# Performance work log

Measured on AMD Instinct MI355X. Metric: run time of the kernel, lower is better.

Reference implementation:

```python
import jax, jax.numpy as jnp
import numpy as np

B, Hc, Wc, C, NH, SR, WS = 4, 64, 64, 256, 8, 2, 4
N = Hc * Wc


def _window_partition(x, ws, H, W):
    # x: (B, h, N, d) -> (B*h*nWin, ws*ws, d)
    Bb, h, _, d = x.shape
    x = x.reshape(Bb * h, H // ws, ws, W // ws, ws, d)
    x = x.transpose(0, 1, 3, 2, 4, 5)
    return x.reshape(-1, ws * ws, d)


def _window_reverse(win, ws, H, W, head):
    nwin = (H // ws) * (W // ws)
    Bh = win.shape[0] // nwin
    x = win.reshape(Bh, H // ws, W // ws, ws, ws, -1).transpose(0, 1, 3, 2, 4, 5).reshape(Bh, H, W, -1)
    Bb = Bh // head
    x = x.reshape(Bb, head, H, W, -1).transpose(0, 2, 3, 1, 4)  # heads interleave into channels
    return x.reshape(Bb, H * W, -1)


def _layernorm(x, w, b):
    m = x.mean(-1, keepdims=True)
    v = x.var(-1, keepdims=True)
    return (x - m) / jnp.sqrt(v + 1e-5) * w + b


def setup_inputs() -> dict:
    key = jax.random.key(0)
    ks = jax.random.split(key, 16)
    lin = lambda k, i, o: 0.02 * jax.random.normal(k, (i, o), jnp.float32)
    inp = {
        'x': jax.random.normal(ks[0], (B, N, C), jnp.float32),
        'q1_w': lin(ks[1], C, C // 2), 'q1_b': jnp.zeros((C // 2,), jnp.float32),
        'kv1_w': lin(ks[2], C, C), 'kv1_b': jnp.zeros((C,), jnp.float32),
        'q2_w': lin(ks[3], C, C // 2), 'q2_b': jnp.zeros((C // 2,), jnp.float32),
        'kv2_w': lin(ks[4], C, C), 'kv2_b': jnp.zeros((C,), jnp.float32),
        'lepe_w': lin(ks[5], C, C), 'lepe_b': jnp.zeros((C,), jnp.float32),
        'lepe_conv_w': jnp.sqrt(2.0 / 9.0) * jax.random.normal(ks[6], (C, 1, 3, 3), jnp.float32),
        'lepe_conv_b': jnp.zeros((C,), jnp.float32),
        'sr_w': jnp.sqrt(2.0 / (SR * SR * C)) * jax.random.normal(ks[7], (C, C, SR, SR), jnp.float32),
        'sr_b': jnp.zeros((C,), jnp.float32),
        'norm_w': jnp.ones((C,), jnp.float32), 'norm_b': jnp.zeros((C,), jnp.float32),
        'proj_w': lin(ks[8], C, C), 'proj_b': jnp.zeros((C,), jnp.float32),
        'H': Hc, 'W': Wc,
    }
    return inp


def reference(x, q1_w, q1_b, kv1_w, kv1_b, q2_w, q2_b, kv2_w, kv2_b,
              lepe_w, lepe_b, lepe_conv_w, lepe_conv_b, sr_w, sr_b,
              norm_w, norm_b, proj_w, proj_b, H, W):
    Bb, Nn, Cc = x.shape
    h2 = NH // 2
    d = Cc // NH
    sr = sr_w.shape[-1]
    scale = d ** -0.5
    ws = WS

    # lepe: linear -> depthwise 3x3 conv
    l = (x @ lepe_w + lepe_b).transpose(0, 2, 1).reshape(Bb, Cc, H, W)
    l = jax.lax.conv_general_dilated(l, lepe_conv_w, (1, 1), ((1, 1), (1, 1)),
                                     dimension_numbers=('NCHW', 'OIHW', 'NCHW'),
                                     feature_group_count=Cc) + lepe_conv_b[None, :, None, None]
    lepe = l.reshape(Bb, Cc, Nn).transpose(0, 2, 1)

    # branch 1: spatial-reduction global attention
    q1 = (x @ q1_w + q1_b).reshape(Bb, Nn, h2, d).transpose(0, 2, 1, 3)
    x_img = x.transpose(0, 2, 1).reshape(Bb, Cc, H, W)
    xs = jax.lax.conv_general_dilated(x_img, sr_w, (sr, sr), 'VALID',
                                      dimension_numbers=('NCHW', 'OIHW', 'NCHW')) + sr_b[None, :, None, None]
    N1 = (H // sr) * (W // sr)
    xs = xs.reshape(Bb, Cc, N1).transpose(0, 2, 1)
    xs = jax.nn.gelu(_layernorm(xs, norm_w, norm_b), approximate=False)
    kv1 = (xs @ kv1_w + kv1_b).reshape(Bb, N1, 2, h2, d).transpose(2, 0, 3, 1, 4)
    k1, v1 = kv1[0], kv1[1]
    attn1 = jax.nn.softmax(jnp.einsum('bhnd,bhmd->bhnm', q1, k1) * scale, axis=-1)
    x1 = jnp.einsum('bhnm,bhmd->bnhd', attn1, v1).reshape(Bb, Nn, Cc // 2)
    g = jax.lax.stop_gradient(attn1).mean(1).mean(1).reshape(Bb, H // sr, W // sr)
    g = jnp.repeat(jnp.repeat(g, sr, axis=1), sr, axis=2)  # nearest upsample to (B,H,W)

    # branch 2: Swin-style windowed attention (window 4)
    q2 = (x @ q2_w + q2_b).reshape(Bb, Nn, h2, d).transpose(0, 2, 1, 3)
    kv2 = (x @ kv2_w + kv2_b).reshape(Bb, Nn, 2, h2, d).transpose(2, 0, 3, 1, 4)
    k2, v2 = kv2[0], kv2[1]
    q2w = _window_partition(q2, ws, H, W)
    k2w = _window_partition(k2, ws, H, W)
    v2w = _window_partition(v2, ws, H, W)
    attn2 = jax.nn.softmax(jnp.einsum('wnd,wmd->wnm', q2w, k2w) * scale, axis=-1)
    x2 = jnp.einsum('wnm,wmd->wnd', attn2, v2w)
    x2 = _window_reverse(x2, ws, H, W, h2)
    nwin = (H // ws) * (W // ws)
    lm = jax.lax.stop_gradient(attn2).reshape(Bb, h2, nwin, ws * ws, ws * ws).mean(1).mean(2)
    lm = lm.reshape(Bb, H // ws, W // ws, ws, ws).transpose(0, 1, 3, 2, 4).reshape(Bb, H, W)

    out = jnp.concatenate([x1, x2], axis=-1)
    p = (out + lepe) @ proj_w + proj_b
    out = p + p  # proj_drop is identity at p=0.0, so x = drop(p) + p = 2p

    mask = lm + g
    mask1 = mask.reshape(Bb, H * W)
    mask2 = mask.transpose(0, 2, 1).reshape(Bb, H * W)
    return out, mask1, mask2
```

## Files before the change

kernel.cpp:

```cpp
#include <hip/hip_runtime.h>
#include <hip/hip_bf16.h>
#include <math.h>

typedef __hip_bfloat16 bf16;
typedef __attribute__((ext_vector_type(8))) short bf16x8;
typedef __attribute__((ext_vector_type(4))) short bf16x4;
typedef __attribute__((ext_vector_type(4))) float f32x4;

__device__ __forceinline__ float b2f(bf16 v) { return __bfloat162float(v); }
__device__ __forceinline__ bf16  f2b(float v) { return __float2bfloat16(v); }
__device__ __forceinline__ float s2f(short v) { return __uint_as_float(((unsigned)(unsigned short)v) << 16); }

__device__ __forceinline__ void gl_lds16(const void* g, void* l)
{
    __builtin_amdgcn_global_load_lds(
        (const __attribute__((address_space(1))) void*)g,
        (__attribute__((address_space(3))) void*)l, 16, 0, 0);
}

__global__ void detect_dtype(const void* x, int* flag)
{
    __shared__ int cnt;
    if (threadIdx.x == 0) cnt = 0;
    __syncthreads();
    const unsigned* w = (const unsigned*)x;
    int sane = 0;
    for (int i = threadIdx.x; i < 2048; i += 256) {
        unsigned lo = (w[i] & 0xFFFFu) << 16;
        float v = __uint_as_float(lo);
        float a = fabsf(v);
        if (v == 0.f || (a > 1e-8f && a < 1e4f)) sane++;
    }
    atomicAdd(&cnt, sane);
    __syncthreads();
    if (threadIdx.x == 0) *flag = (cnt < 1640) ? 1 : 0;
}

struct AllArgs {
    const void* x; bf16* cx;
    const void* srw;  bf16* srwT;
    const void* dww;  bf16* dwT;
    const void* psrc[10]; bf16* pdst[10]; int pn[10];
    const void* wsrc[6]; bf16* wdst[6]; int wN[6]; int wblkoff[7];
    float* gbuf;
};
__global__ void convert_all(AllArgs a, const int* __restrict__ flag)
{
    int blk = blockIdx.x, t = threadIdx.x;
    int fl = *flag;
    if (blk < 4096) {
        int i = blk * 256 + t;
        if (fl) {
            float4 v = ((const float4*)a.x)[i];
            bf16 tmp[4];
            tmp[0] = f2b(v.x); tmp[1] = f2b(v.y); tmp[2] = f2b(v.z); tmp[3] = f2b(v.w);
            *(bf16x4*)&a.cx[i * 4] = *(bf16x4*)tmp;
        } else {
            ((bf16x4*)a.cx)[i] = ((const bf16x4*)a.x)[i];
        }
    } else if (blk < 5120) {
        int o = (blk - 4096) * 256 + t;
        int co = o >> 10, kg = o & 1023;
        int e = kg >> 8, ci = kg & 255;
        int si = co * 1024 + ci * 4 + e;
        float v = fl ? ((const float*)a.srw)[si] : s2f(((const short*)a.srw)[si]);
        a.srwT[o] = f2b(v);
    } else if (blk < 5129) {
        int o = (blk - 5120) * 256 + t;
        if (o >= 2304) return;
        int k = o >> 8, c = o & 255;
        float v = fl ? ((const float*)a.dww)[c * 9 + k] : s2f(((const short*)a.dww)[c * 9 + k]);
        a.dwT[o] = f2b(v);
    } else if (blk < 5139) {
        int bi = blk - 5129;
        int n = a.pn[bi];
        const void* s = a.psrc[bi];
        bf16* d = a.pdst[bi];
        for (int i = t; i < n; i += 256)
            d[i] = fl ? f2b(((const float*)s)[i]) : f2b(s2f(((const short*)s)[i]));
    } else if (blk < 6419) {
        int wblk = blk - 5139;
        int ti = 0;
        while (wblk >= a.wblkoff[ti + 1]) ++ti;
        int o = (wblk - a.wblkoff[ti]) * 256 + t;
        int n = o >> 8, k = o & 255;
        int N = a.wN[ti];
        float v = fl ? ((const float*)a.wsrc[ti])[k * N + n]
                     : s2f(((const short*)a.wsrc[ti])[k * N + n]);
        a.wdst[ti][o] = f2b(v);
    } else {
        for (int i = t; i < 4096; i += 256) a.gbuf[i] = 0.f;
    }
}

__device__ __forceinline__ void qkv_body(
    int bx, int by, char* smem,
    const bf16* __restrict__ A, const bf16* __restrict__ WT, const bf16* __restrict__ bias,
    bf16* __restrict__ Cl, bf16* __restrict__ Cq1, bf16* __restrict__ Cq2, bf16* __restrict__ Ckv2)
{
    char* As = smem;
    char* Bs = smem + 8192;
    int t = threadIdx.x;
    int m0 = bx * 128, ybase = by * 128;
    int w = t >> 6, l = t & 63, lane16 = l & 15, quad = l >> 4;
    int wr = w >> 1, wc = w & 1;

    int oph0 = w * 2048 + l * 16;
    int oph1 = oph0 + 1024;
    int olog0 = oph0 ^ (((oph0 >> 7) & 3) << 4);
    int olog1 = oph1 ^ (((oph1 >> 7) & 3) << 4);
    int row0 = olog0 >> 6, ce0 = (olog0 & 63) >> 1;
    int row1 = olog1 >> 6, ce1 = (olog1 & 63) >> 1;
    char* asb0 = As + w * 2048; char* asb1 = asb0 + 1024;
    char* bsb0 = Bs + w * 2048; char* bsb1 = bsb0 + 1024;

    f32x4 acc[4][4] = {};
    for (int k0 = 0; k0 < 256; k0 += 32) {
        gl_lds16(&A[(size_t)(m0 + row0) * 256 + k0 + ce0], asb0);
        gl_lds16(&A[(size_t)(m0 + row1) * 256 + k0 + ce1], asb1);
        gl_lds16(&WT[(size_t)(ybase + row0) * 256 + k0 + ce0], bsb0);
        gl_lds16(&WT[(size_t)(ybase + row1) * 256 + k0 + ce1], bsb1);
        __syncthreads();
        bf16x8 a[4], b[4];
        #pragma unroll
        for (int i = 0; i < 4; ++i) {
            int ra = wr * 64 + i * 16 + lane16;
            int oa = (ra << 6) + (quad << 4);
            oa ^= (((oa >> 7) & 3) << 4);
            a[i] = *(const bf16x8*)(As + oa);
            int rb = wc * 64 + i * 16 + lane16;
            int ob = (rb << 6) + (quad << 4);
            ob ^= (((ob >> 7) & 3) << 4);
            b[i] = *(const bf16x8*)(Bs + ob);
        }
        #pragma unroll
        for (int i = 0; i < 4; ++i)
            #pragma unroll
            for (int j = 0; j < 4; ++j)
                acc[i][j] = __builtin_amdgcn_mfma_f32_16x16x32_bf16(a[i], b[j], acc[i][j], 0, 0, 0);
        __syncthreads();
    }
    bf16* C; int N, cbase;
    if (ybase < 256)      { C = Cl;   N = 256; cbase = ybase; }
    else if (ybase < 384) { C = Cq1;  N = 128; cbase = ybase - 256; }
    else if (ybase < 512) { C = Cq2;  N = 128; cbase = ybase - 384; }
    else                  { C = Ckv2; N = 256; cbase = ybase - 512; }
    float mult = (ybase >= 256 && ybase < 512)
               ? (0.17677669529663687f * 1.4426950408889634f) : 1.f;
    #pragma unroll
    for (int j = 0; j < 4; ++j) {
        int gcol = ybase + wc * 64 + j * 16 + lane16;
        float bv = b2f(bias[gcol]);
        int col = cbase + wc * 64 + j * 16 + lane16;
        #pragma unroll
        for (int i = 0; i < 4; ++i)
            #pragma unroll
            for (int r = 0; r < 4; ++r) {
                int row = m0 + wr * 64 + i * 16 + quad * 4 + r;
                C[(size_t)row * N + col] = f2b((acc[i][j][r] + bv) * mult);
            }
    }
}

__device__ __forceinline__ void sr_body(
    int bx, int by, char* smem,
    const bf16* __restrict__ x, const bf16* __restrict__ WT,
    const bf16* __restrict__ bias, bf16* __restrict__ C)
{
    bf16 (*As)[40] = (bf16(*)[40])smem;
    bf16 (*Bs)[40] = (bf16(*)[40])(smem + 5120);
    int t = threadIdx.x;
    int m0 = bx * 64, n0 = by * 64;
    int w = t >> 6, l = t & 63, lane16 = l & 15, quad = l >> 4;
    int sr = t >> 2, sc = (t & 3) * 8;
    int brow = m0 + sr;
    int b = brow >> 10, p = brow & 1023;
    int pi = p >> 5, pj = p & 31;
    f32x4 acc[4] = {};
    for (int k0 = 0; k0 < 1024; k0 += 32) {
        int kg = k0 + sc;
        int e = kg >> 8, ci = kg & 255;
        int di = e >> 1, dj = e & 1;
        int n = (2 * pi + di) * 64 + 2 * pj + dj;
        *(bf16x8*)&As[sr][sc] = *(const bf16x8*)&x[(size_t)((b << 12) + n) * 256 + ci];
        *(bf16x8*)&Bs[sr][sc] = *(const bf16x8*)&WT[(size_t)(n0 + sr) * 1024 + kg];
        __syncthreads();
        bf16x8 a = *(const bf16x8*)&As[w * 16 + lane16][quad * 8];
        #pragma unroll
        for (int ct = 0; ct < 4; ++ct) {
            bf16x8 bb = *(const bf16x8*)&Bs[ct * 16 + lane16][quad * 8];
            acc[ct] = __builtin_amdgcn_mfma_f32_16x16x32_bf16(a, bb, acc[ct], 0, 0, 0);
        }
        __syncthreads();
    }
    #pragma unroll
    for (int ct = 0; ct < 4; ++ct) {
        int col = n0 + ct * 16 + lane16;
        float bv = b2f(bias[col]);
        #pragma unroll
        for (int r = 0; r < 4; ++r) {
            int row = m0 + w * 16 + quad * 4 + r;
            C[(size_t)row * 256 + col] = f2b(acc[ct][r] + bv);
        }
    }
}

__global__ __launch_bounds__(256) void fuseA(
    const bf16* __restrict__ cx, const bf16* __restrict__ wTqkv, const bf16* __restrict__ bcat,
    bf16* __restrict__ Cl, bf16* __restrict__ Cq1, bf16* __restrict__ Cq2, bf16* __restrict__ Ckv2,
    const bf16* __restrict__ srwT, const bf16* __restrict__ srb, bf16* __restrict__ xs_pre)
{
    __shared__ __align__(16) char smem[16384];
    int idx = blockIdx.x;
    int g = idx >> 2, r3 = idx & 3;
    if (r3 < 3) {
        int q = g * 3 + r3;
        qkv_body(q & 127, q >> 7, smem, cx, wTqkv, bcat, Cl, Cq1, Cq2, Ckv2);
    } else {
        sr_body(g & 63, g >> 6, smem, cx, srwT, srb, xs_pre);
    }
}

__device__ __forceinline__ void ln_body(
    int blk,
    const bf16* __restrict__ xin, const bf16* __restrict__ nw,
    const bf16* __restrict__ nb, bf16* __restrict__ xout)
{
    int w = threadIdx.x >> 6, lane = threadIdx.x & 63;
    int r = blk * 4 + w;
    bf16x4 xv = *(const bf16x4*)&xin[(size_t)r * 256 + lane * 4];
    float v[4];
    #pragma unroll
    for (int j = 0; j < 4; ++j) v[j] = s2f(xv[j]);
    float s = v[0] + v[1] + v[2] + v[3];
    #pragma unroll
    for (int o = 1; o <= 32; o <<= 1) s += __shfl_xor(s, o);
    float mean = s * (1.f / 256.f);
    float ss = 0.f;
    #pragma unroll
    for (int j = 0; j < 4; ++j) { float d = v[j] - mean; ss += d * d; }
    #pragma unroll
    for (int o = 1; o <= 32; o <<= 1) ss += __shfl_xor(ss, o);
    float inv = rsqrtf(ss * (1.f / 256.f) + 1e-5f);
    bf16x4 wv = *(const bf16x4*)&nw[lane * 4];
    bf16x4 bv = *(const bf16x4*)&nb[lane * 4];
    bf16 ov[4];
    #pragma unroll
    for (int j = 0; j < 4; ++j) {
        float y = (v[j] - mean) * inv * s2f(wv[j]) + s2f(bv[j]);
        ov[j] = f2b(0.5f * y * (1.f + erff(y * 0.70710678118654752f)));
    }
    *(bf16x4*)&xout[(size_t)r * 256 + lane * 4] = *(bf16x4*)ov;
}

__device__ __forceinline__ void dw_body(
    int blk,
    const bf16* __restrict__ lin, const bf16* __restrict__ dwT,
    const bf16* __restrict__ bias, bf16* __restrict__ out)
{
    int tid = blk * 256 + threadIdx.x;
    int c0 = (tid & 31) * 8;
    int j  = (tid >> 5) & 63;
    int i  = ((tid >> 11) & 31) * 2;
    int b  = tid >> 16;
    float acc0[8], acc1[8];
    bf16x8 bv = *(const bf16x8*)&bias[c0];
    #pragma unroll
    for (int q = 0; q < 8; ++q) { acc0[q] = s2f(bv[q]); acc1[q] = s2f(bv[q]); }
    bf16x8 wv[3][3];
    #pragma unroll
    for (int di = 0; di < 3; ++di)
        #pragma unroll
        for (int dj = 0; dj < 3; ++dj)
            wv[di][dj] = *(const bf16x8*)&dwT[(di * 3 + dj) * 256 + c0];
    #pragma unroll
    for (int r = -1; r <= 2; ++r) {
        int ii = i + r;
        if (ii < 0 || ii > 63) continue;
        #pragma unroll
        for (int dj = 0; dj < 3; ++dj) {
            int jj = j + dj - 1;
            if (jj < 0 || jj > 63) continue;
            bf16x8 xv = *(const bf16x8*)&lin[(size_t)((b << 12) + ii * 64 + jj) * 256 + c0];
            if (r <= 1) {
                bf16x8 w0 = wv[r + 1][dj];
                #pragma unroll
                for (int q = 0; q < 8; ++q) acc0[q] += s2f(xv[q]) * s2f(w0[q]);
            }
            if (r >= 0) {
                bf16x8 w1 = wv[r][dj];
                #pragma unroll
                for (int q = 0; q < 8; ++q) acc1[q] += s2f(xv[q]) * s2f(w1[q]);
            }
        }
    }
    bf16 ov[8];
    #pragma unroll
    for (int q = 0; q < 8; ++q) ov[q] = f2b(acc0[q]);
    *(bf16x8*)&out[(size_t)((b << 12) + i * 64 + j) * 256 + c0] = *(bf16x8*)ov;
    #pragma unroll
    for (int q = 0; q < 8; ++q) ov[q] = f2b(acc1[q]);
    *(bf16x8*)&out[(size_t)((b << 12) + (i + 1) * 64 + j) * 256 + c0] = *(bf16x8*)ov;
}

__global__ __launch_bounds__(256) void fuseB(
    const bf16* __restrict__ xs_pre, const bf16* __restrict__ nw,
    const bf16* __restrict__ nb, bf16* __restrict__ xs,
    const bf16* __restrict__ lepe_lin, const bf16* __restrict__ dwT,
    const bf16* __restrict__ dwb, bf16* __restrict__ lepe)
{
    int idx = blockIdx.x;
    if ((idx & 1) == 0) ln_body(idx >> 1, xs_pre, nw, nb, xs);
    else                dw_body(idx >> 1, lepe_lin, dwT, dwb, lepe);
}

__global__ __launch_bounds__(256) void gemm_kv1(
    const bf16* __restrict__ A, const bf16* __restrict__ WT, const bf16* __restrict__ bias,
    bf16* __restrict__ k1, bf16* __restrict__ v1T)
{
    __shared__ bf16 As[64][40];
    __shared__ bf16 Bs[64][40];
    int t = threadIdx.x;
    int m0 = blockIdx.x * 64, n0 = blockIdx.y * 64;
    int w = t >> 6, l = t & 63, lane16 = l & 15, quad = l >> 4;
    int sr = t >> 2, sc = (t & 3) * 8;
    f32x4 acc[4] = {};
    for (int k0 = 0; k0 < 256; k0 += 32) {
        *(bf16x8*)&As[sr][sc] = *(const bf16x8*)&A[(size_t)(m0 + sr) * 256 + k0 + sc];
        *(bf16x8*)&Bs[sr][sc] = *(const bf16x8*)&WT[(size_t)(n0 + sr) * 256 + k0 + sc];
        __syncthreads();
        bf16x8 a = *(const bf16x8*)&As[w * 16 + lane16][quad * 8];
        #pragma unroll
        for (int ct = 0; ct < 4; ++ct) {
            bf16x8 b = *(const bf16x8*)&Bs[ct * 16 + lane16][quad * 8];
            acc[ct] = __builtin_amdgcn_mfma_f32_16x16x32_bf16(a, b, acc[ct], 0, 0, 0);
        }
        __syncthreads();
    }
    #pragma unroll
    for (int ct = 0; ct < 4; ++ct) {
        int col = n0 + ct * 16 + lane16;
        float bv = b2f(bias[col]);
        #pragma unroll
        for (int r = 0; r < 4; ++r) {
            int row = m0 + w * 16 + quad * 4 + r;
            float val = acc[ct][r] + bv;
            int bb = row >> 10, key = row & 1023;
            if (col < 128) {
                k1[(size_t)row * 128 + col] = f2b(val);
            } else {
                int h = (col - 128) >> 5, ch = (col - 128) & 31;
                v1T[(size_t)((bb * 4 + h) * 32 + ch) * 1024 + key] = f2b(val);
            }
        }
    }
}

__global__ __launch_bounds__(256) void attn1_split(
    const bf16* __restrict__ q1, const bf16* __restrict__ k1,
    const bf16* __restrict__ v1T, bf16* __restrict__ attn_out, float* __restrict__ g)
{
    __shared__ bf16 Kt[2][64][40];
    __shared__ bf16 Vt[2][32][68];
    __shared__ bf16 PTT[4][16][68];
    __shared__ float gp[1024];

    int t = threadIdx.x;
    int blk = blockIdx.x;
    int qc = blk & 63, h = (blk >> 6) & 3, b = blk >> 8;
    int n0 = qc * 64;
    int w = t >> 6, l = t & 63, lane16 = l & 15, quad = l >> 4;

    const bf16* Kbase = k1 + (size_t)b * 1024 * 128 + 32 * h;
    const bf16* Vbase = v1T + (size_t)((b * 4 + h) * 32) * 1024;
    bf16x8 qa = *(const bf16x8*)&q1[(size_t)(b * 4096 + n0 + 16 * w + lane16) * 128 + 32 * h + quad * 8];

    for (int i = t; i < 1024; i += 256) gp[i] = 0.f;

    int sr = t >> 2, sc = (t & 3) * 8;
    int vrow = t >> 3, vcol = (t & 7) * 8;
    bf16* ptt = &PTT[w][0][0];

    *(bf16x8*)&Kt[0][sr][sc]     = *(const bf16x8*)&Kbase[(size_t)sr * 128 + sc];
    *(bf16x8*)&Vt[0][vrow][vcol] = *(const bf16x8*)&Vbase[(size_t)vrow * 1024 + vcol];
    __syncthreads();

    float lacc = 0.f;
    f32x4 oT0 = {}, oT1 = {};

    for (int ktl = 0; ktl < 16; ++ktl) {
        int cur = ktl & 1;
        bf16x8 knext, vnext;
        if (ktl < 15) {
            knext = *(const bf16x8*)&Kbase[(size_t)((ktl + 1) * 64 + sr) * 128 + sc];
            vnext = *(const bf16x8*)&Vbase[(size_t)vrow * 1024 + (ktl + 1) * 64 + vcol];
        }
        bf16x8 kf[4];
        #pragma unroll
        for (int st = 0; st < 4; ++st)
            kf[st] = *(const bf16x8*)&Kt[cur][st * 16 + lane16][quad * 8];
        #pragma unroll
        for (int st = 0; st < 4; ++st) {
            f32x4 z = {0.f, 0.f, 0.f, 0.f};
            f32x4 sT = __builtin_amdgcn_mfma_f32_16x16x32_bf16(kf[st], qa, z, 0, 0, 0);
            bf16 pk[4];
            #pragma unroll
            for (int r = 0; r < 4; ++r) {
                float p = exp2f(sT[r]);
                lacc += p;
                pk[r] = f2b(p);
            }
            *(bf16x4*)&ptt[lane16 * 68 + st * 16 + quad * 4] = *(bf16x4*)pk;
        }
        #pragma unroll
        for (int kh = 0; kh < 2; ++kh) {
            bf16x8 pf  = *(const bf16x8*)&ptt[lane16 * 68 + kh * 32 + quad * 8];
            bf16x8 vf0 = *(const bf16x8*)&Vt[cur][lane16][kh * 32 + quad * 8];
            bf16x8 vf1 = *(const bf16x8*)&Vt[cur][16 + lane16][kh * 32 + quad * 8];
            oT0 = __builtin_amdgcn_mfma_f32_16x16x32_bf16(vf0, pf, oT0, 0, 0, 0);
            oT1 = __builtin_amdgcn_mfma_f32_16x16x32_bf16(vf1, pf, oT1, 0, 0, 0);
        }
        if (ktl < 15) {
            *(bf16x8*)&Kt[cur ^ 1][sr][sc]     = knext;
            *(bf16x8*)&Vt[cur ^ 1][vrow][vcol] = vnext;
        }
        __syncthreads();
    }

    lacc += __shfl_xor(lacc, 16);
    lacc += __shfl_xor(lacc, 32);
    float rl = 1.f / lacc;
    {
        bf16 ov0[4], ov1[4];
        #pragma unroll
        for (int r = 0; r < 4; ++r) {
            ov0[r] = f2b(oT0[r] * rl);
            ov1[r] = f2b(oT1[r] * rl);
        }
        size_t ro = (size_t)(b * 4096 + n0 + 16 * w + lane16) * 256 + 32 * h;
        *(bf16x4*)&attn_out[ro + quad * 4]      = *(bf16x4*)ov0;
        *(bf16x4*)&attn_out[ro + 16 + quad * 4] = *(bf16x4*)ov1;
    }

    float rlq[4];
    #pragma unroll
    for (int r = 0; r < 4; ++r) rlq[r] = __shfl(rl, quad * 4 + r);

    *(bf16x8*)&Kt[0][sr][sc] = *(const bf16x8*)&Kbase[(size_t)sr * 128 + sc];
    __syncthreads();
    for (int ktl = 0; ktl < 16; ++ktl) {
        int cur = ktl & 1;
        bf16x8 knext;
        if (ktl < 15)
            knext = *(const bf16x8*)&Kbase[(size_t)((ktl + 1) * 64 + sr) * 128 + sc];
        bf16x8 kf2[4];
        #pragma unroll
        for (int st = 0; st < 4; ++st)
            kf2[st] = *(const bf16x8*)&Kt[cur][st * 16 + lane16][quad * 8];
        #pragma unroll
        for (int st = 0; st < 4; ++st) {
            f32x4 z = {0.f, 0.f, 0.f, 0.f};
            f32x4 s = __builtin_amdgcn_mfma_f32_16x16x32_bf16(qa, kf2[st], z, 0, 0, 0);
            float cs = 0.f;
            #pragma unroll
            for (int r = 0; r < 4; ++r) cs += exp2f(s[r]) * rlq[r];
            cs += __shfl_xor(cs, 16);
            cs += __shfl_xor(cs, 32);
            if (quad == 0) atomicAdd(&gp[ktl * 64 + st * 16 + lane16], cs);
        }
        if (ktl < 15)
            *(bf16x8*)&Kt[cur ^ 1][sr][sc] = knext;
        __syncthreads();
    }

    for (int i = t; i < 1024; i += 256)
        atomicAdd(&g[(b << 10) + i], gp[i] * (1.f / 16384.f));
}

__global__ __launch_bounds__(256) void attn2_mfma(
    const bf16* __restrict__ q2, const bf16* __restrict__ kv2,
    bf16* __restrict__ attn_out, float* __restrict__ lm)
{
    __shared__ bf16 PT2[4][16 * 40];
    __shared__ float lmw[16];
    int t = threadIdx.x;
    int blk = blockIdx.x;
    int b = blk >> 8, win = blk & 255;
    int wi = win >> 4, wj = win & 15;
    int h = t >> 6, l = t & 63, lane16 = l & 15, quad = l >> 4;

    if (t < 16) lmw[t] = 0.f;
    bf16* ptt = &PT2[h][0];
    {
        bf16 zz[4] = {};
        *(bf16x4*)&ptt[lane16 * 40 + 16 + quad * 4] = *(bf16x4*)zz;
    }
    __syncthreads();

    size_t base = (size_t)(b * 4096);
    int r0 = wi * 4, c0w = wj * 4;
    int tq = (r0 + (lane16 >> 2)) * 64 + c0w + (lane16 & 3);

    bf16x8 qa = *(const bf16x8*)&q2[(base + tq) * 128 + h * 32 + quad * 8];
    bf16x8 kf = *(const bf16x8*)&kv2[(base + tq) * 256 + h * 32 + quad * 8];

    f32x4 z = {0.f, 0.f, 0.f, 0.f};
    f32x4 sT = __builtin_amdgcn_mfma_f32_16x16x32_bf16(kf, qa, z, 0, 0, 0);
    float sv[4];
    #pragma unroll
    for (int r = 0; r < 4; ++r) sv[r] = sT[r];
    float mx = fmaxf(fmaxf(sv[0], sv[1]), fmaxf(sv[2], sv[3]));
    mx = fmaxf(mx, __shfl_xor(mx, 16));
    mx = fmaxf(mx, __shfl_xor(mx, 32));
    float p[4], lsum = 0.f;
    #pragma unroll
    for (int r = 0; r < 4; ++r) { p[r] = exp2f(sv[r] - mx); lsum += p[r]; }
    lsum += __shfl_xor(lsum, 16);
    lsum += __shfl_xor(lsum, 32);
    float rl = 1.f / lsum;
    bf16 pk[4];
    #pragma unroll
    for (int r = 0; r < 4; ++r) { p[r] *= rl; pk[r] = f2b(p[r]); }
    *(bf16x4*)&ptt[lane16 * 40 + quad * 4] = *(bf16x4*)pk;

    bf16x8 vf0 = {}, vf1 = {};
    if (quad < 2) {
        #pragma unroll
        for (int jj = 0; jj < 8; ++jj) {
            int key = quad * 8 + jj;
            int tk = (r0 + (key >> 2)) * 64 + c0w + (key & 3);
            const short* vp = (const short*)&kv2[(base + tk) * 256 + 128 + h * 32];
            vf0[jj] = vp[lane16];
            vf1[jj] = vp[16 + lane16];
        }
    }
    bf16x8 pf = *(const bf16x8*)&ptt[lane16 * 40 + quad * 8];
    f32x4 o0 = __builtin_amdgcn_mfma_f32_16x16x32_bf16(vf0, pf, z, 0, 0, 0);
    f32x4 o1 = __builtin_amdgcn_mfma_f32_16x16x32_bf16(vf1, pf, z, 0, 0, 0);
    {
        bf16 ov0[4], ov1[4];
        #pragma unroll
        for (int r = 0; r < 4; ++r) { ov0[r] = f2b(o0[r]); ov1[r] = f2b(o1[r]); }
        bf16* op = attn_out + (base + tq) * 256 + 128 + h * 32;
        *(bf16x4*)&op[quad * 4]      = *(bf16x4*)ov0;
        *(bf16x4*)&op[16 + quad * 4] = *(bf16x4*)ov1;
    }

    #pragma unroll
    for (int r = 0; r < 4; ++r) {
        float c = p[r];
        c += __shfl_xor(c, 1);
        c += __shfl_xor(c, 2);
        c += __shfl_xor(c, 4);
        c += __shfl_xor(c, 8);
        if (lane16 == 0) atomicAdd(&lmw[quad * 4 + r], c);
    }
    __syncthreads();
    if (t < 16) {
        int nk = (r0 + (t >> 2)) * 64 + c0w + (t & 3);
        lm[(b << 12) + nk] = lmw[t] * (1.f / 64.f);
    }
}

__global__ __launch_bounds__(256) void gemm_proj128(
    const bf16* __restrict__ A, const bf16* __restrict__ A2,
    const bf16* __restrict__ WT, const bf16* __restrict__ bias,
    const float* __restrict__ lm, const float* __restrict__ g,
    void* __restrict__ dout, const int* __restrict__ flag)
{
    if (blockIdx.y == 2) {
        if (blockIdx.x >= 64) return;
        int tid = blockIdx.x * 256 + threadIdx.x;
        int b = tid >> 12, n = tid & 4095;
        int i = n >> 6, j = n & 63;
        float v = lm[tid] + g[(b << 10) + (i >> 1) * 32 + (j >> 1)];
        size_t o1 = (size_t)4194304 + (b << 12) + i * 64 + j;
        size_t o2 = (size_t)4194304 + 16384 + (b << 12) + j * 64 + i;
        if (*flag) { ((float*)dout)[o1] = v; ((float*)dout)[o2] = v; }
        else       { ((bf16*)dout)[o1] = f2b(v); ((bf16*)dout)[o2] = f2b(v); }
        return;
    }
    __shared__ bf16 As[128][40];
    __shared__ bf16 Bs[128][40];
    int t = threadIdx.x;
    int m0 = blockIdx.x * 128, n0 = blockIdx.y * 128;
    int w = t >> 6, l = t & 63, lane16 = l & 15, quad = l >> 4;
    int wr = w >> 1, wc = w & 1;
    int sr = t >> 1, sc = (t & 1) * 16;
    f32x4 acc[4][4] = {};
    for (int k0 = 0; k0 < 256; k0 += 32) {
        #pragma unroll
        for (int hh = 0; hh < 2; ++hh) {
            bf16x8 va = *(const bf16x8*)&A[(size_t)(m0 + sr) * 256 + k0 + sc + hh * 8];
            bf16x8 vb = *(const bf16x8*)&A2[(size_t)(m0 + sr) * 256 + k0 + sc + hh * 8];
            bf16 tmp[8];
            #pragma unroll
            for (int q = 0; q < 8; ++q) tmp[q] = f2b(s2f(va[q]) + s2f(vb[q]));
            *(bf16x8*)&As[sr][sc + hh * 8] = *(bf16x8*)tmp;
        }
        *(bf16x8*)&Bs[sr][sc]     = *(const bf16x8*)&WT[(size_t)(n0 + sr) * 256 + k0 + sc];
        *(bf16x8*)&Bs[sr][sc + 8] = *(const bf16x8*)&WT[(size_t)(n0 + sr) * 256 + k0 + sc + 8];
        __syncthreads();
        bf16x8 a[4], b[4];
        #pragma unroll
        for (int i = 0; i < 4; ++i) {
            a[i] = *(const bf16x8*)&As[wr * 64 + i * 16 + lane16][quad * 8];
            b[i] = *(const bf16x8*)&Bs[wc * 64 + i * 16 + lane16][quad * 8];
        }
        #pragma unroll
        for (int i = 0; i < 4; ++i)
            #pragma unroll
            for (int j = 0; j < 4; ++j)
                acc[i][j] = __builtin_amdgcn_mfma_f32_16x16x32_bf16(a[i], b[j], acc[i][j], 0, 0, 0);
        __syncthreads();
    }
    #pragma unroll
    for (int j = 0; j < 4; ++j) {
        int col = n0 + wc * 64 + j * 16 + lane16;
        float bv = b2f(bias[col]);
        #pragma unroll
        for (int i = 0; i < 4; ++i)
            #pragma unroll
            for (int r = 0; r < 4; ++r) {
                int row = m0 + wr * 64 + i * 16 + quad * 4 + r;
                float rv = (acc[i][j][r] + bv) * 2.f;
                size_t o = (size_t)row * 256 + col;
                if (*flag) ((float*)dout)[o] = rv;
                else       ((bf16*)dout)[o] = f2b(rv);
            }
    }
}

extern "C" void kernel_launch(void* const* d_in, const int* in_sizes, int n_in,
                              void* d_out, int out_size, void* d_ws, size_t ws_size,
                              hipStream_t stream)
{
    char* ws = (char*)d_ws;
    size_t off = 0;
    auto alloc = [&](size_t bytes) {
        void* p = ws + off;
        off += (bytes + 255) & ~(size_t)255;
        return p;
    };
    bf16* cx       = (bf16*)alloc((size_t)4194304 * 2);
    bf16* lepe_lin = (bf16*)alloc((size_t)4194304 * 2);
    bf16* attn_out = lepe_lin;
    bf16* lepe     = (bf16*)alloc((size_t)4194304 * 2);
    bf16* q1buf    = (bf16*)alloc((size_t)2097152 * 2);
    bf16* q2buf    = (bf16*)alloc((size_t)2097152 * 2);
    bf16* kv2buf   = (bf16*)alloc((size_t)4194304 * 2);
    bf16* xs_pre   = (bf16*)alloc((size_t)1048576 * 2);
    bf16* k1buf    = xs_pre;
    bf16* v1Tbuf   = xs_pre + 524288;
    bf16* xs       = (bf16*)alloc((size_t)1048576 * 2);
    bf16* wTqkv    = (bf16*)alloc((size_t)196608 * 2);
    bf16* kv1_wT   = (bf16*)alloc(65536 * 2);
    bf16* proj_wT  = (bf16*)alloc(65536 * 2);
    bf16* sr_wT    = (bf16*)alloc(262144 * 2);
    bf16* dwT      = (bf16*)alloc(2304 * 2);
    bf16* bcat     = (bf16*)alloc(768 * 2);
    bf16* ckv1b    = (bf16*)alloc(256 * 2);
    bf16* csrb     = (bf16*)alloc(256 * 2);
    bf16* cnw      = (bf16*)alloc(256 * 2);
    bf16* cnb      = (bf16*)alloc(256 * 2);
    bf16* cpb      = (bf16*)alloc(256 * 2);
    bf16* clcb     = (bf16*)alloc(256 * 2);
    float* gbuf    = (float*)alloc(4096 * 4);
    float* lmbuf   = (float*)alloc(16384 * 4);
    int*   flag    = (int*)alloc(256);

    detect_dtype<<<1, 256, 0, stream>>>(d_in[0], flag);

    AllArgs aa;
    aa.x = d_in[0]; aa.cx = cx;
    aa.srw = d_in[13]; aa.srwT = sr_wT;
    aa.dww = d_in[11]; aa.dwT = dwT;
    aa.psrc[0] = d_in[10]; aa.pdst[0] = bcat;       aa.pn[0] = 256;
    aa.psrc[1] = d_in[2];  aa.pdst[1] = bcat + 256; aa.pn[1] = 128;
    aa.psrc[2] = d_in[6];  aa.pdst[2] = bcat + 384; aa.pn[2] = 128;
    aa.psrc[3] = d_in[8];  aa.pdst[3] = bcat + 512; aa.pn[3] = 256;
    aa.psrc[4] = d_in[4];  aa.pdst[4] = ckv1b;      aa.pn[4] = 256;
    aa.psrc[5] = d_in[14]; aa.pdst[5] = csrb;       aa.pn[5] = 256;
    aa.psrc[6] = d_in[15]; aa.pdst[6] = cnw;        aa.pn[6] = 256;
    aa.psrc[7] = d_in[16]; aa.pdst[7] = cnb;        aa.pn[7] = 256;
    aa.psrc[8] = d_in[18]; aa.pdst[8] = cpb;        aa.pn[8] = 256;
    aa.psrc[9] = d_in[12]; aa.pdst[9] = clcb;       aa.pn[9] = 256;
    aa.wsrc[0] = d_in[9];  aa.wdst[0] = wTqkv;             aa.wN[0] = 256;
    aa.wsrc[1] = d_in[1];  aa.wdst[1] = wTqkv + 256 * 256; aa.wN[1] = 128;
    aa.wsrc[2] = d_in[5];  aa.wdst[2] = wTqkv + 384 * 256; aa.wN[2] = 128;
    aa.wsrc[3] = d_in[7];  aa.wdst[3] = wTqkv + 512 * 256; aa.wN[3] = 256;
    aa.wsrc[4] = d_in[3];  aa.wdst[4] = kv1_wT;            aa.wN[4] = 256;
    aa.wsrc[5] = d_in[17]; aa.wdst[5] = proj_wT;           aa.wN[5] = 256;
    int bo[7] = {0, 256, 384, 512, 768, 1024, 1280};
    for (int i = 0; i < 7; ++i) aa.wblkoff[i] = bo[i];
    aa.gbuf = gbuf;
    convert_all<<<6420, 256, 0, stream>>>(aa, flag);

    fuseA<<<1024, 256, 0, stream>>>(cx, wTqkv, bcat, lepe_lin, q1buf, q2buf, kv2buf,
                                    sr_wT, csrb, xs_pre);
    fuseB<<<2048, 256, 0, stream>>>(xs_pre, cnw, cnb, xs, lepe_lin, dwT, clcb, lepe);
    gemm_kv1<<<dim3(64, 4), 256, 0, stream>>>(xs, kv1_wT, ckv1b, k1buf, v1Tbuf);
    attn1_split<<<1024, 256, 0, stream>>>(q1buf, k1buf, v1Tbuf, attn_out, gbuf);
    attn2_mfma<<<1024, 256, 0, stream>>>(q2buf, kv2buf, attn_out, lmbuf);
    gemm_proj128<<<dim3(128, 3), 256, 0, stream>>>(attn_out, lepe, proj_wT, cpb,
                                                   lmbuf, gbuf, d_out, flag);
}
```

Baseline: 259.1 us.

## Use padded LDS for A tiles, shuffle P via registers, drop log2e prescale

The QKV GEMM now stages the A tile through registers into a padded LDS layout instead of direct global-to-LDS loads. Attention 1 passes P fragments between lanes with shuffles instead of writing them to and reading them back from an LDS scratch buffer. The softmax scale no longer folds in log2(e), and exp2f is swapped for __expf at all three sites. The intent is to cut LDS traffic and barriers in attention, but the register-staged A loads may add latency in the GEMM.

```diff
diff --git a/kernel.cpp b/kernel.cpp
--- a/kernel.cpp
+++ b/kernel.cpp
@@ -98,12 +98,13 @@
     const bf16* __restrict__ A, const bf16* __restrict__ WT, const bf16* __restrict__ bias,
     bf16* __restrict__ Cl, bf16* __restrict__ Cq1, bf16* __restrict__ Cq2, bf16* __restrict__ Ckv2)
 {
-    char* As = smem;
-    char* Bs = smem + 8192;
+    bf16 (*As)[40] = (bf16(*)[40])smem;
+    char* Bs = smem + 10240;
     int t = threadIdx.x;
     int m0 = bx * 128, ybase = by * 128;
     int w = t >> 6, l = t & 63, lane16 = l & 15, quad = l >> 4;
     int wr = w >> 1, wc = w & 1;
+    int srow = t >> 1, scol = (t & 1) * 16;
 
     int oph0 = w * 2048 + l * 16;
     int oph1 = oph0 + 1024;
@@ -111,23 +112,19 @@
     int olog1 = oph1 ^ (((oph1 >> 7) & 3) << 4);
     int row0 = olog0 >> 6, ce0 = (olog0 & 63) >> 1;
     int row1 = olog1 >> 6, ce1 = (olog1 & 63) >> 1;
-    char* asb0 = As + w * 2048; char* asb1 = asb0 + 1024;
     char* bsb0 = Bs + w * 2048; char* bsb1 = bsb0 + 1024;
 
     f32x4 acc[4][4] = {};
     for (int k0 = 0; k0 < 256; k0 += 32) {
-        gl_lds16(&A[(size_t)(m0 + row0) * 256 + k0 + ce0], asb0);
-        gl_lds16(&A[(size_t)(m0 + row1) * 256 + k0 + ce1], asb1);
+        *(bf16x8*)&As[srow][scol]     = *(const bf16x8*)&A[(size_t)(m0 + srow) * 256 + k0 + scol];
+        *(bf16x8*)&As[srow][scol + 8] = *(const bf16x8*)&A[(size_t)(m0 + srow) * 256 + k0 + scol + 8];
         gl_lds16(&WT[(size_t)(ybase + row0) * 256 + k0 + ce0], bsb0);
         gl_lds16(&WT[(size_t)(ybase + row1) * 256 + k0 + ce1], bsb1);
         __syncthreads();
         bf16x8 a[4], b[4];
         #pragma unroll
         for (int i = 0; i < 4; ++i) {
-            int ra = wr * 64 + i * 16 + lane16;
-            int oa = (ra << 6) + (quad << 4);
-            oa ^= (((oa >> 7) & 3) << 4);
-            a[i] = *(const bf16x8*)(As + oa);
+            a[i] = *(const bf16x8*)&As[wr * 64 + i * 16 + lane16][quad * 8];
             int rb = wc * 64 + i * 16 + lane16;
             int ob = (rb << 6) + (quad << 4);
             ob ^= (((ob >> 7) & 3) << 4);
@@ -145,8 +142,7 @@
     else if (ybase < 384) { C = Cq1;  N = 128; cbase = ybase - 256; }
     else if (ybase < 512) { C = Cq2;  N = 128; cbase = ybase - 384; }
     else                  { C = Ckv2; N = 256; cbase = ybase - 512; }
-    float mult = (ybase >= 256 && ybase < 512)
-               ? (0.17677669529663687f * 1.4426950408889634f) : 1.f;
+    float mult = (ybase >= 256 && ybase < 512) ? 0.17677669529663687f : 1.f;
     #pragma unroll
     for (int j = 0; j < 4; ++j) {
         int gcol = ybase + wc * 64 + j * 16 + lane16;
@@ -210,7 +206,7 @@
     bf16* __restrict__ Cl, bf16* __restrict__ Cq1, bf16* __restrict__ Cq2, bf16* __restrict__ Ckv2,
     const bf16* __restrict__ srwT, const bf16* __restrict__ srb, bf16* __restrict__ xs_pre)
 {
-    __shared__ __align__(16) char smem[16384];
+    __shared__ __align__(16) char smem[18432];
     int idx = blockIdx.x;
     int g = idx >> 2, r3 = idx & 3;
     if (r3 < 3) {
@@ -362,7 +358,6 @@
 {
     __shared__ bf16 Kt[2][64][40];
     __shared__ bf16 Vt[2][32][68];
-    __shared__ bf16 PTT[4][16][68];
     __shared__ float gp[1024];
 
     int t = threadIdx.x;
@@ -379,7 +374,10 @@
 
     int sr = t >> 2, sc = (t & 3) * 8;
     int vrow = t >> 3, vcol = (t & 7) * 8;
-    bf16* ptt = &PTT[w][0][0];
+
+    int s0 = lane16 + 32 * (quad & 1);
+    int s1 = s0 + 16;
+    int sel = quad >> 1;
 
     *(bf16x8*)&Kt[0][sr][sc]     = *(const bf16x8*)&Kbase[(size_t)sr * 128 + sc];
     *(bf16x8*)&Vt[0][vrow][vcol] = *(const bf16x8*)&Vbase[(size_t)vrow * 1024 + vcol];
@@ -399,6 +397,7 @@
         #pragma unroll
         for (int st = 0; st < 4; ++st)
             kf[st] = *(const bf16x8*)&Kt[cur][st * 16 + lane16][quad * 8];
+        unsigned b01[4], b23[4];
         #pragma unroll
         for (int st = 0; st < 4; ++st) {
             f32x4 z = {0.f, 0.f, 0.f, 0.f};
@@ -406,15 +405,27 @@
             bf16 pk[4];
             #pragma unroll
             for (int r = 0; r < 4; ++r) {
-                float p = exp2f(sT[r]);
+                float p = __expf(sT[r]);
                 lacc += p;
                 pk[r] = f2b(p);
             }
-            *(bf16x4*)&ptt[lane16 * 68 + st * 16 + quad * 4] = *(bf16x4*)pk;
+            unsigned u0 = *(unsigned short*)&pk[0];
+            unsigned u1 = *(unsigned short*)&pk[1];
+            unsigned u2 = *(unsigned short*)&pk[2];
+            unsigned u3 = *(unsigned short*)&pk[3];
+            b01[st] = u0 | (u1 << 16);
+            b23[st] = u2 | (u3 << 16);
         }
         #pragma unroll
         for (int kh = 0; kh < 2; ++kh) {
-            bf16x8 pf  = *(const bf16x8*)&ptt[lane16 * 68 + kh * 32 + quad * 8];
+            unsigned c01 = sel ? b01[2 * kh + 1] : b01[2 * kh];
+            unsigned c23 = sel ? b23[2 * kh + 1] : b23[2 * kh];
+            unsigned wrds[4];
+            wrds[0] = (unsigned)__shfl((int)c01, s0);
+            wrds[1] = (unsigned)__shfl((int)c23, s0);
+            wrds[2] = (unsigned)__shfl((int)c01, s1);
+            wrds[3] = (unsigned)__shfl((int)c23, s1);
+            bf16x8 pf = *(bf16x8*)wrds;
             bf16x8 vf0 = *(const bf16x8*)&Vt[cur][lane16][kh * 32 + quad * 8];
             bf16x8 vf1 = *(const bf16x8*)&Vt[cur][16 + lane16][kh * 32 + quad * 8];
             oT0 = __builtin_amdgcn_mfma_f32_16x16x32_bf16(vf0, pf, oT0, 0, 0, 0);
@@ -463,7 +474,7 @@
             f32x4 s = __builtin_amdgcn_mfma_f32_16x16x32_bf16(qa, kf2[st], z, 0, 0, 0);
             float cs = 0.f;
             #pragma unroll
-            for (int r = 0; r < 4; ++r) cs += exp2f(s[r]) * rlq[r];
+            for (int r = 0; r < 4; ++r) cs += __expf(s[r]) * rlq[r];
             cs += __shfl_xor(cs, 16);
             cs += __shfl_xor(cs, 32);
             if (quad == 0) atomicAdd(&gp[ktl * 64 + st * 16 + lane16], cs);
@@ -514,7 +525,7 @@
     mx = fmaxf(mx, __shfl_xor(mx, 32));
     float p[4], lsum = 0.f;
     #pragma unroll
-    for (int r = 0; r < 4; ++r) { p[r] = exp2f(sv[r] - mx); lsum += p[r]; }
+    for (int r = 0; r < 4; ++r) { p[r] = __expf(sv[r] - mx); lsum += p[r]; }
     lsum += __shfl_xor(lsum, 16);
     lsum += __shfl_xor(lsum, 32);
     float rl = 1.f / lsum;
```

Result: faster. 249.1 us (-3.9%).
